# Optimization experiments

Hardware: AMD Instinct MI355X
Metric: run time of the kernel (lower is better)

Reference implementation:

```python
import jax, jax.numpy as jnp
import numpy as np

B, L, H, E, D = 2, 2048, 8, 64, 64


def setup_inputs() -> dict:
    key = jax.random.key(0)
    k0, k1, k2, k3 = jax.random.split(key, 4)
    u = jax.random.normal(k0, (B, L, H, D), dtype=jnp.float32)
    q = jax.random.normal(k1, (B, L, H, E), dtype=jnp.float32)
    k = jax.random.normal(k2, (B, L, H, E), dtype=jnp.float32)
    v = jax.random.normal(k3, (B, L, H, D), dtype=jnp.float32)
    # causal mask: True where attention is DISALLOWED (strict upper triangle)
    attn_mask = jnp.triu(jnp.ones((L, L), dtype=bool), k=1)[None, None]  # (1,1,L,L)
    return {"u": u, "q": q, "k": k, "v": v, "attn_mask": attn_mask}


def reference(u, q, k, v, attn_mask):
    # q,k: [B,L,H,E]; v,u: [B,L,H,D]; attn_mask: [1,1,L,S] bool (True = masked)
    Edim = q.shape[-1]
    S = k.shape[1]
    scale = 1.0 / np.sqrt(Edim)
    scores = jnp.einsum('blhe,bshe->bhls', q, k)  # [B,H,L,S]
    x = jax.nn.relu(scale * scores)
    # attention_normalize(method='squared_relu'): relu(x)^2 / seq_len; masked -> 0
    A = jnp.where(attn_mask, 0.0, x * x) / S  # [B,H,L,S]
    # dropout is identity in eval mode
    V = u * jnp.einsum('bhls,bshd->blhd', A, v)  # [B,L,H,D]
    return V
```

## Files before the change

### kernel.cpp

```cpp
#include <hip/hip_runtime.h>
#include <hip/hip_bf16.h>

namespace {
constexpr int Lc = 2048, Hc = 8;
constexpr int RS = Hc * 64;
constexpr int NKT = 32;
constexpr int TILE_BYTES = 16384;
}

typedef __attribute__((ext_vector_type(8))) short bf16x8;
typedef __attribute__((ext_vector_type(16))) float f32x16;
typedef unsigned int u32;
typedef __attribute__((ext_vector_type(4))) u32 u32x4;

__device__ __forceinline__ u32 bfu(float x) {
    return (u32)__builtin_bit_cast(unsigned short, __float2bfloat16(x));
}
__device__ __forceinline__ short f2bf(float x) {
    return (short)__builtin_bit_cast(unsigned short, __float2bfloat16(x));
}

#define MFMA32(a, b, c) __builtin_amdgcn_mfma_f32_32x32x16_bf16((a), (b), (c), 0, 0, 0)

#define GLL16(gp, lp) __builtin_amdgcn_global_load_lds( \
    (const __attribute__((address_space(1))) unsigned int*)(gp), \
    (__attribute__((address_space(3))) unsigned int*)(lp), 16, 0, 0)

__global__ __launch_bounds__(256)
void prep_kv(const float* __restrict__ kg, const float* __restrict__ vg,
             short* __restrict__ ws)
{
    const int kt = blockIdx.x, bh = blockIdx.y;
    const int b = bh >> 3, h = bh & 7;
    const size_t base = ((size_t)b * Lc * Hc + h) * 64;
    char* tile = (char*)ws + (size_t)(bh * NKT + kt) * TILE_BYTES;
    const int tid = threadIdx.x;

    {
        const int c = tid & 7, e0 = c * 8;
        #pragma unroll
        for (int p = 0; p < 2; ++p) {
            const int s = (tid >> 3) + 32 * p;
            const float* src = kg + base + (size_t)(kt * 64 + s) * RS + e0;
            float4 x0 = *(const float4*)src;
            float4 x1 = *(const float4*)(src + 4);
            bf16x8 w = { f2bf(x0.x), f2bf(x0.y), f2bf(x0.z), f2bf(x0.w),
                         f2bf(x1.x), f2bf(x1.y), f2bf(x1.z), f2bf(x1.w) };
            const int lane = (c & 1) * 32 + (s & 31);
            const int byte = ((s >> 5) * 4 + (c >> 1)) * 1024 + lane * 16;
            *(bf16x8*)(tile + byte) = w;
        }
    }
    {
        const int d = tid & 63;
        #pragma unroll
        for (int p = 0; p < 2; ++p) {
            const int sblk = (tid >> 6) + 4 * p;
            const int s0 = sblk * 8;
            float xv[8];
            #pragma unroll
            for (int j = 0; j < 8; ++j)
                xv[j] = vg[base + (size_t)(kt * 64 + s0 + j) * RS + d];
            bf16x8 w = { f2bf(xv[0]), f2bf(xv[1]), f2bf(xv[2]), f2bf(xv[3]),
                         f2bf(xv[4]), f2bf(xv[5]), f2bf(xv[6]), f2bf(xv[7]) };
            const int lane = (sblk & 1) * 32 + (d & 31);
            const int byte = 8192 + ((d >> 5) * 4 + (sblk >> 1)) * 1024 + lane * 16;
            *(bf16x8*)(tile + byte) = w;
        }
    }
}

__global__ __launch_bounds__(256, 2)
void gate_attn(const float* __restrict__ ug, const float* __restrict__ qg,
               const short* __restrict__ ws, float* __restrict__ outg)
{
    __shared__ __align__(16) char lds[2][2 * TILE_BYTES];

    const int tid = threadIdx.x;
    const int wave = tid >> 6, lane = tid & 63;
    const int col = lane & 31, hi = lane >> 5;
    const int qs = wave & 1, ktp = wave >> 1;

    const int i = (int)blockIdx.x;
    const int xcd = i & 7, w = i >> 3;
    const int bh = 2 * xcd + (w >= 32 ? 1 : 0);
    const int x = w & 31;
    const int strip = (w < 32) ? (31 - x) : x;

    const int b = bh >> 3, h = bh & 7;
    const size_t base = ((size_t)b * Lc * Hc + h) * 64;
    const char* wsbh = (const char*)ws + (size_t)bh * NKT * TILE_BYTES;

    const int IT = ((strip + 1) + 1) >> 1;
    const int qw = strip * 64 + qs * 32;
    const int qg_l = qw + col;

    bf16x8 qf[4];
    #pragma unroll
    for (int es = 0; es < 4; ++es) {
        const float* p = qg + base + (size_t)(qw + col) * RS + es * 16 + hi * 8;
        float4 a = *(const float4*)p;
        float4 c2 = *(const float4*)(p + 4);
        qf[es] = (bf16x8){ f2bf(a.x),  f2bf(a.y),  f2bf(a.z),  f2bf(a.w),
                           f2bf(c2.x), f2bf(c2.y), f2bf(c2.z), f2bf(c2.w) };
    }

    auto STAGEG = [&](int t0, int buf) {
        #pragma unroll
        for (int t = 0; t < 2; ++t) {
            if (t0 + t <= strip) {
                const char* src = wsbh + (size_t)(t0 + t) * TILE_BYTES + tid * 16;
                char* dst = &lds[buf][t * TILE_BYTES] + tid * 16;
                #pragma unroll
                for (int j = 0; j < 4; ++j)
                    GLL16(src + j * 4096, dst + j * 4096);
            }
        }
    };

    f32x16 oacc[2];
    #pragma unroll
    for (int r = 0; r < 16; ++r) { oacc[0][r] = 0.f; oacc[1][r] = 0.f; }

    STAGEG(0, 0);
    __syncthreads();

    for (int it = 0; it < IT; ++it) {
        if (it + 1 < IT) STAGEG(2 * (it + 1), (it & 1) ^ 1);
        const int kt = 2 * it + ktp;
        if (kt <= strip) {
            const char* kb = &lds[it & 1][ktp * TILE_BYTES];

            f32x16 sacc[2];
            #pragma unroll
            for (int r = 0; r < 16; ++r) { sacc[0][r] = 0.f; sacc[1][r] = 0.f; }
            __builtin_amdgcn_s_setprio(1);
            #pragma unroll
            for (int sb = 0; sb < 2; ++sb)
                #pragma unroll
                for (int es = 0; es < 4; ++es) {
                    bf16x8 kf = *(const bf16x8*)(kb + (sb * 4 + es) * 1024 + lane * 16);
                    sacc[sb] = MFMA32(kf, qf[es], sacc[sb]);
                }
            __builtin_amdgcn_s_setprio(0);

            const bool dmask = (kt == strip);
            u32 pa[4][4];
            #pragma unroll
            for (int sb = 0; sb < 2; ++sb) {
                float pv[16];
                #pragma unroll
                for (int r = 0; r < 16; ++r) {
                    float x2 = sacc[sb][r];
                    x2 = (x2 > 0.f) ? x2 * x2 : 0.f;
                    const int s_g = kt * 64 + sb * 32 + (r & 3) + 8 * (r >> 2) + 4 * hi;
                    if (dmask && s_g > qg_l) x2 = 0.f;
                    pv[r] = x2;
                }
                u32 W[8];
                #pragma unroll
                for (int t = 0; t < 8; ++t)
                    W[t] = bfu(pv[2 * t]) | (bfu(pv[2 * t + 1]) << 16);
                asm volatile("v_permlane32_swap_b32 %0, %1" : "+v"(W[0]), "+v"(W[2]));
                asm volatile("v_permlane32_swap_b32 %0, %1" : "+v"(W[1]), "+v"(W[3]));
                asm volatile("v_permlane32_swap_b32 %0, %1" : "+v"(W[4]), "+v"(W[6]));
                asm volatile("v_permlane32_swap_b32 %0, %1" : "+v"(W[5]), "+v"(W[7]));
                pa[sb * 2 + 0][0] = W[0]; pa[sb * 2 + 0][1] = W[1];
                pa[sb * 2 + 0][2] = W[2]; pa[sb * 2 + 0][3] = W[3];
                pa[sb * 2 + 1][0] = W[4]; pa[sb * 2 + 1][1] = W[5];
                pa[sb * 2 + 1][2] = W[6]; pa[sb * 2 + 1][3] = W[7];
            }

            const char* vb = kb + 8192;
            __builtin_amdgcn_s_setprio(1);
            #pragma unroll
            for (int dh = 0; dh < 2; ++dh)
                #pragma unroll
                for (int ks = 0; ks < 4; ++ks) {
                    bf16x8 vf = *(const bf16x8*)(vb + (dh * 4 + ks) * 1024 + lane * 16);
                    u32x4 pw = { pa[ks][0], pa[ks][1], pa[ks][2], pa[ks][3] };
                    oacc[dh] = MFMA32(__builtin_bit_cast(bf16x8, pw), vf, oacc[dh]);
                }
            __builtin_amdgcn_s_setprio(0);
        }
        __syncthreads();
    }

    float* red = (float*)&lds[0][0];
    if (ktp == 0) {
        #pragma unroll
        for (int dh = 0; dh < 2; ++dh)
            #pragma unroll
            for (int r = 0; r < 16; ++r) {
                const int m = (r & 3) + 8 * (r >> 2) + 4 * hi;
                red[(qs * 32 + m) * 64 + dh * 32 + col] = oacc[dh][r];
            }
    }
    __syncthreads();
    if (ktp == 1) {
        const float sc = 1.0f / (64.0f * 2048.0f);
        #pragma unroll
        for (int dh = 0; dh < 2; ++dh)
            #pragma unroll
            for (int r = 0; r < 16; ++r) {
                const int m = (r & 3) + 8 * (r >> 2) + 4 * hi;
                const float o = oacc[dh][r] + red[(qs * 32 + m) * 64 + dh * 32 + col];
                const size_t idx = base + (size_t)(qw + m) * RS + dh * 32 + col;
                outg[idx] = ug[idx] * o * sc;
            }
    }
}

extern "C" void kernel_launch(void* const* d_in, const int* in_sizes, int n_in,
                              void* d_out, int out_size, void* d_ws, size_t ws_size,
                              hipStream_t stream) {
    const float* u = (const float*)d_in[0];
    const float* q = (const float*)d_in[1];
    const float* k = (const float*)d_in[2];
    const float* v = (const float*)d_in[3];
    float* out = (float*)d_out;

    prep_kv<<<dim3(NKT, 16), dim3(256), 0, stream>>>(k, v, (short*)d_ws);
    gate_attn<<<dim3(512), dim3(256), 0, stream>>>(u, q, (const short*)d_ws, out);
}
```

Before: 36.03 us.

## Split key range across blocks with atomic accumulation for balanced causal work

Replaces the per-strip block (with two waves splitting key tiles and reducing through LDS) by a split-K scheme. Each 128-thread block handles a chunk of at most eight key tiles for one query strip, and partial outputs are combined with float atomicAdd into a buffer zeroed by a new kernel. This is meant to balance the causal triangle's uneven work across 1280 smaller blocks and improve occupancy. It also swaps the bf16 packing for v_cvt_pk_bf16_f32, and in exchange adds an extra zeroing launch, atomic traffic, and a non-deterministic summation order.

```diff
diff --git a/kernel.cpp b/kernel.cpp
--- a/kernel.cpp
+++ b/kernel.cpp
@@ -6,6 +6,7 @@
 constexpr int RS = Hc * 64;
 constexpr int NKT = 32;
 constexpr int TILE_BYTES = 16384;
+constexpr int OUT4 = 2 * Lc * Hc * 64 / 4;
 }
 
 typedef __attribute__((ext_vector_type(8))) short bf16x8;
@@ -13,9 +14,6 @@
 typedef unsigned int u32;
 typedef __attribute__((ext_vector_type(4))) u32 u32x4;
 
-__device__ __forceinline__ u32 bfu(float x) {
-    return (u32)__builtin_bit_cast(unsigned short, __float2bfloat16(x));
-}
 __device__ __forceinline__ short f2bf(float x) {
     return (short)__builtin_bit_cast(unsigned short, __float2bfloat16(x));
 }
@@ -25,6 +23,11 @@
 #define GLL16(gp, lp) __builtin_amdgcn_global_load_lds( \
     (const __attribute__((address_space(1))) unsigned int*)(gp), \
     (__attribute__((address_space(3))) unsigned int*)(lp), 16, 0, 0)
+
+__global__ __launch_bounds__(256) void zero_out(float4* __restrict__ o) {
+    const int i = blockIdx.x * 256 + threadIdx.x;
+    if (i < OUT4) o[i] = make_float4(0.f, 0.f, 0.f, 0.f);
+}
 
 __global__ __launch_bounds__(256)
 void prep_kv(const float* __restrict__ kg, const float* __restrict__ vg,
@@ -70,28 +73,42 @@
     }
 }
 
-__global__ __launch_bounds__(256, 2)
+__global__ __launch_bounds__(128, 2)
 void gate_attn(const float* __restrict__ ug, const float* __restrict__ qg,
                const short* __restrict__ ws, float* __restrict__ outg)
 {
-    __shared__ __align__(16) char lds[2][2 * TILE_BYTES];
+    __shared__ __align__(16) char lds[2][TILE_BYTES];
 
     const int tid = threadIdx.x;
-    const int wave = tid >> 6, lane = tid & 63;
+    const int qs = tid >> 6, lane = tid & 63;
     const int col = lane & 31, hi = lane >> 5;
-    const int qs = wave & 1, ktp = wave >> 1;
 
     const int i = (int)blockIdx.x;
-    const int xcd = i & 7, w = i >> 3;
-    const int bh = 2 * xcd + (w >= 32 ? 1 : 0);
-    const int x = w & 31;
-    const int strip = (w < 32) ? (31 - x) : x;
-
+    const int xcd = i & 7;
+    const int j = i >> 3;
+    const int bh_bit = j & 1;
+    const int c = j >> 1;
+    int strip = 0, k0 = 0, k1 = 0;
+    {
+        int acc = 0;
+        for (int s = 31; s >= 0; --s) {
+            const int cc = (s + 8) >> 3;
+            if (c < acc + cc) {
+                strip = s;
+                const int ci = c - acc;
+                const int per = (s + cc) / cc;
+                k0 = ci * per;
+                k1 = min(k0 + per - 1, s);
+                break;
+            }
+            acc += cc;
+        }
+    }
+    const int bh = 2 * xcd + bh_bit;
     const int b = bh >> 3, h = bh & 7;
     const size_t base = ((size_t)b * Lc * Hc + h) * 64;
     const char* wsbh = (const char*)ws + (size_t)bh * NKT * TILE_BYTES;
 
-    const int IT = ((strip + 1) + 1) >> 1;
     const int qw = strip * 64 + qs * 32;
     const int qg_l = qw + col;
 
@@ -105,110 +122,91 @@
                            f2bf(c2.x), f2bf(c2.y), f2bf(c2.z), f2bf(c2.w) };
     }
 
-    auto STAGEG = [&](int t0, int buf) {
-        #pragma unroll
-        for (int t = 0; t < 2; ++t) {
-            if (t0 + t <= strip) {
-                const char* src = wsbh + (size_t)(t0 + t) * TILE_BYTES + tid * 16;
-                char* dst = &lds[buf][t * TILE_BYTES] + tid * 16;
-                #pragma unroll
-                for (int j = 0; j < 4; ++j)
-                    GLL16(src + j * 4096, dst + j * 4096);
-            }
-        }
+    auto STAGE = [&](int t, int buf) {
+        const char* src = wsbh + (size_t)t * TILE_BYTES + tid * 16;
+        char* dst = &lds[buf][0] + tid * 16;
+        #pragma unroll
+        for (int ii = 0; ii < 8; ++ii)
+            GLL16(src + ii * 2048, dst + ii * 2048);
     };
 
     f32x16 oacc[2];
     #pragma unroll
     for (int r = 0; r < 16; ++r) { oacc[0][r] = 0.f; oacc[1][r] = 0.f; }
 
-    STAGEG(0, 0);
+    STAGE(k0, 0);
     __syncthreads();
 
-    for (int it = 0; it < IT; ++it) {
-        if (it + 1 < IT) STAGEG(2 * (it + 1), (it & 1) ^ 1);
-        const int kt = 2 * it + ktp;
-        if (kt <= strip) {
-            const char* kb = &lds[it & 1][ktp * TILE_BYTES];
-
-            f32x16 sacc[2];
-            #pragma unroll
-            for (int r = 0; r < 16; ++r) { sacc[0][r] = 0.f; sacc[1][r] = 0.f; }
-            __builtin_amdgcn_s_setprio(1);
-            #pragma unroll
-            for (int sb = 0; sb < 2; ++sb)
-                #pragma unroll
-                for (int es = 0; es < 4; ++es) {
-                    bf16x8 kf = *(const bf16x8*)(kb + (sb * 4 + es) * 1024 + lane * 16);
-                    sacc[sb] = MFMA32(kf, qf[es], sacc[sb]);
-                }
-            __builtin_amdgcn_s_setprio(0);
-
-            const bool dmask = (kt == strip);
-            u32 pa[4][4];
-            #pragma unroll
-            for (int sb = 0; sb < 2; ++sb) {
-                float pv[16];
-                #pragma unroll
-                for (int r = 0; r < 16; ++r) {
-                    float x2 = sacc[sb][r];
-                    x2 = (x2 > 0.f) ? x2 * x2 : 0.f;
-                    const int s_g = kt * 64 + sb * 32 + (r & 3) + 8 * (r >> 2) + 4 * hi;
-                    if (dmask && s_g > qg_l) x2 = 0.f;
-                    pv[r] = x2;
-                }
-                u32 W[8];
-                #pragma unroll
-                for (int t = 0; t < 8; ++t)
-                    W[t] = bfu(pv[2 * t]) | (bfu(pv[2 * t + 1]) << 16);
-                asm volatile("v_permlane32_swap_b32 %0, %1" : "+v"(W[0]), "+v"(W[2]));
-                asm volatile("v_permlane32_swap_b32 %0, %1" : "+v"(W[1]), "+v"(W[3]));
-                asm volatile("v_permlane32_swap_b32 %0, %1" : "+v"(W[4]), "+v"(W[6]));
-                asm volatile("v_permlane32_swap_b32 %0, %1" : "+v"(W[5]), "+v"(W[7]));
-                pa[sb * 2 + 0][0] = W[0]; pa[sb * 2 + 0][1] = W[1];
-                pa[sb * 2 + 0][2] = W[2]; pa[sb * 2 + 0][3] = W[3];
-                pa[sb * 2 + 1][0] = W[4]; pa[sb * 2 + 1][1] = W[5];
-                pa[sb * 2 + 1][2] = W[6]; pa[sb * 2 + 1][3] = W[7];
-            }
-
-            const char* vb = kb + 8192;
-            __builtin_amdgcn_s_setprio(1);
-            #pragma unroll
-            for (int dh = 0; dh < 2; ++dh)
-                #pragma unroll
-                for (int ks = 0; ks < 4; ++ks) {
-                    bf16x8 vf = *(const bf16x8*)(vb + (dh * 4 + ks) * 1024 + lane * 16);
-                    u32x4 pw = { pa[ks][0], pa[ks][1], pa[ks][2], pa[ks][3] };
-                    oacc[dh] = MFMA32(__builtin_bit_cast(bf16x8, pw), vf, oacc[dh]);
-                }
-            __builtin_amdgcn_s_setprio(0);
-        }
+    for (int kt = k0; kt <= k1; ++kt) {
+        const int buf = (kt - k0) & 1;
+        if (kt < k1) STAGE(kt + 1, buf ^ 1);
+        const char* kb = &lds[buf][0];
+
+        f32x16 sacc[2];
+        #pragma unroll
+        for (int r = 0; r < 16; ++r) { sacc[0][r] = 0.f; sacc[1][r] = 0.f; }
+        __builtin_amdgcn_s_setprio(1);
+        #pragma unroll
+        for (int sb = 0; sb < 2; ++sb)
+            #pragma unroll
+            for (int es = 0; es < 4; ++es) {
+                bf16x8 kf = *(const bf16x8*)(kb + (sb * 4 + es) * 1024 + lane * 16);
+                sacc[sb] = MFMA32(kf, qf[es], sacc[sb]);
+            }
+        __builtin_amdgcn_s_setprio(0);
+
+        const bool dmask = (kt == strip);
+        u32 pa[4][4];
+        #pragma unroll
+        for (int sb = 0; sb < 2; ++sb) {
+            float pv[16];
+            #pragma unroll
+            for (int r = 0; r < 16; ++r) {
+                float x2 = sacc[sb][r];
+                x2 = (x2 > 0.f) ? x2 * x2 : 0.f;
+                const int s_g = kt * 64 + sb * 32 + (r & 3) + 8 * (r >> 2) + 4 * hi;
+                if (dmask && s_g > qg_l) x2 = 0.f;
+                pv[r] = x2;
+            }
+            u32 W[8];
+            #pragma unroll
+            for (int t = 0; t < 8; ++t)
+                asm("v_cvt_pk_bf16_f32 %0, %1, %2"
+                    : "=v"(W[t]) : "v"(pv[2 * t]), "v"(pv[2 * t + 1]));
+            asm volatile("v_permlane32_swap_b32 %0, %1" : "+v"(W[0]), "+v"(W[2]));
+            asm volatile("v_permlane32_swap_b32 %0, %1" : "+v"(W[1]), "+v"(W[3]));
+            asm volatile("v_permlane32_swap_b32 %0, %1" : "+v"(W[4]), "+v"(W[6]));
+            asm volatile("v_permlane32_swap_b32 %0, %1" : "+v"(W[5]), "+v"(W[7]));
+            pa[sb * 2 + 0][0] = W[0]; pa[sb * 2 + 0][1] = W[1];
+            pa[sb * 2 + 0][2] = W[2]; pa[sb * 2 + 0][3] = W[3];
+            pa[sb * 2 + 1][0] = W[4]; pa[sb * 2 + 1][1] = W[5];
+            pa[sb * 2 + 1][2] = W[6]; pa[sb * 2 + 1][3] = W[7];
+        }
+
+        const char* vb = kb + 8192;
+        __builtin_amdgcn_s_setprio(1);
+        #pragma unroll
+        for (int dh = 0; dh < 2; ++dh)
+            #pragma unroll
+            for (int ks = 0; ks < 4; ++ks) {
+                bf16x8 vf = *(const bf16x8*)(vb + (dh * 4 + ks) * 1024 + lane * 16);
+                u32x4 pw = { pa[ks][0], pa[ks][1], pa[ks][2], pa[ks][3] };
+                oacc[dh] = MFMA32(__builtin_bit_cast(bf16x8, pw), vf, oacc[dh]);
+            }
+        __builtin_amdgcn_s_setprio(0);
+
         __syncthreads();
     }
 
-    float* red = (float*)&lds[0][0];
-    if (ktp == 0) {
-        #pragma unroll
-        for (int dh = 0; dh < 2; ++dh)
-            #pragma unroll
-            for (int r = 0; r < 16; ++r) {
-                const int m = (r & 3) + 8 * (r >> 2) + 4 * hi;
-                red[(qs * 32 + m) * 64 + dh * 32 + col] = oacc[dh][r];
-            }
-    }
-    __syncthreads();
-    if (ktp == 1) {
-        const float sc = 1.0f / (64.0f * 2048.0f);
-        #pragma unroll
-        for (int dh = 0; dh < 2; ++dh)
-            #pragma unroll
-            for (int r = 0; r < 16; ++r) {
-                const int m = (r & 3) + 8 * (r >> 2) + 4 * hi;
-                const float o = oacc[dh][r] + red[(qs * 32 + m) * 64 + dh * 32 + col];
-                const size_t idx = base + (size_t)(qw + m) * RS + dh * 32 + col;
-                outg[idx] = ug[idx] * o * sc;
-            }
-    }
+    const float sc = 1.0f / (64.0f * 2048.0f);
+    #pragma unroll
+    for (int dh = 0; dh < 2; ++dh)
+        #pragma unroll
+        for (int r = 0; r < 16; ++r) {
+            const int m = (r & 3) + 8 * (r >> 2) + 4 * hi;
+            const size_t idx = base + (size_t)(qw + m) * RS + dh * 32 + col;
+            atomicAdd(&outg[idx], ug[idx] * oacc[dh][r] * sc);
+        }
 }
 
 extern "C" void kernel_launch(void* const* d_in, const int* in_sizes, int n_in,
@@ -220,6 +218,7 @@
     const float* v = (const float*)d_in[3];
     float* out = (float*)d_out;
 
+    zero_out<<<dim3((OUT4 + 255) / 256), dim3(256), 0, stream>>>((float4*)out);
     prep_kv<<<dim3(NKT, 16), dim3(256), 0, stream>>>(k, v, (short*)d_ws);
-    gate_attn<<<dim3(512), dim3(256), 0, stream>>>(u, q, (const short*)d_ws, out);
-}
+    gate_attn<<<dim3(1280), dim3(128), 0, stream>>>(u, q, (const short*)d_ws, out);
+}
```

New measurement: 65.91 us. +82.9%, slower.
